# Performance work log

Hardware: AMD Instinct MI355X
Metric: run time of the kernel (lower is better)

The kernel has to match this reference:

```python
import jax, jax.numpy as jnp
import numpy as np

B, T, H = 2, 2048, 1024
NH = 16
HD = H // NH


def setup_inputs() -> dict:
    key = jax.random.key(0)
    ks = jax.random.split(key, 9)
    s = 0.02
    return {
        "x": jax.random.normal(ks[0], (B, T, H), dtype=jnp.float32),
        "attn_mask": jnp.ones((B, T), dtype=jnp.int32),
        "Wq": jax.random.normal(ks[1], (H, H), dtype=jnp.float32) * s,
        "bq": jnp.zeros((H,), dtype=jnp.float32),
        "Wk": jax.random.normal(ks[2], (H, H), dtype=jnp.float32) * s,
        "bk": jnp.zeros((H,), dtype=jnp.float32),
        "Wv": jax.random.normal(ks[3], (H, H), dtype=jnp.float32) * s,
        "bv": jnp.zeros((H,), dtype=jnp.float32),
        "Wo": jax.random.normal(ks[4], (H, H), dtype=jnp.float32) * s,
        "bo": jnp.zeros((H,), dtype=jnp.float32),
    }


def reference(x, attn_mask, Wq, bq, Wk, bk, Wv, bv, Wo, bo):
    Bc, Tc, Hc = x.shape
    scale = HD ** -0.5
    # projections; torch Linear: y = x @ W.T + b (here W stored as [in,out])
    q = (x @ Wq + bq).reshape(Bc, Tc, NH, HD).transpose(0, 2, 1, 3)  # [B,NH,T,HD]
    k = (x @ Wk + bk).reshape(Bc, Tc, NH, HD).transpose(0, 2, 1, 3)
    v = (x @ Wv + bv).reshape(Bc, Tc, NH, HD).transpose(0, 2, 1, 3)
    scores = jnp.einsum('bhqd,bhkd->bhqk', q, k) * scale  # [B,NH,T,T]
    mask = attn_mask.reshape(Bc, 1, 1, Tc)
    scores = jnp.where(mask == 0, jnp.float32(-jnp.inf), scores)
    probs = jax.nn.softmax(scores, axis=-1)
    ctx = jnp.einsum('bhqk,bhkd->bhqd', probs, v)  # [B,NH,T,HD]
    ctx = ctx.transpose(0, 2, 1, 3).reshape(Bc, Tc, Hc)
    out = ctx @ Wo + bo
    return out
```

## Files before the change

### kernel.cpp

```cpp
#include <hip/hip_runtime.h>

typedef _Float16 f16;
typedef _Float16 f16x8 __attribute__((ext_vector_type(8)));
typedef _Float16 f16x4 __attribute__((ext_vector_type(4)));
typedef __fp16 h16x2 __attribute__((ext_vector_type(2)));
typedef float f32x4 __attribute__((ext_vector_type(4)));

#define MFMA32(a, b, c) __builtin_amdgcn_mfma_f32_16x16x32_f16((a), (b), (c), 0, 0, 0)

static constexpr int Bb = 2, T = 2048, H = 1024, NH = 16, HD = 64;
static constexpr int M = Bb * T;
static constexpr int NQKV = 3 * H;
#define QSCALE 0.1803368801111f

__device__ __forceinline__ void gload_lds16(const void* g, void* l) {
  __builtin_amdgcn_global_load_lds(
      (const __attribute__((address_space(1))) void*)g,
      (__attribute__((address_space(3))) void*)l, 16, 0, 0);
}

__global__ __launch_bounds__(256) void pack_all(const float* __restrict__ x,
                                                const float* __restrict__ Wq,
                                                const float* __restrict__ Wk,
                                                const float* __restrict__ Wv,
                                                const float* __restrict__ Wo,
                                                const float* __restrict__ bq,
                                                const float* __restrict__ bk,
                                                const float* __restrict__ bv,
                                                const int* __restrict__ mask,
                                                f16* __restrict__ xh,
                                                f16* __restrict__ WqkvT,
                                                f16* __restrict__ WoT,
                                                float* __restrict__ bqkv,
                                                float* __restrict__ maskf) {
  __shared__ f16 tile[64][65];
  const int bid = blockIdx.x;
  if (bid < 4096) {
    int i = bid * 256 + threadIdx.x;
    float4 v = ((const float4*)x)[i];
    f16x4 o;
    o[0] = (f16)v.x; o[1] = (f16)v.y; o[2] = (f16)v.z; o[3] = (f16)v.w;
    *(f16x4*)(xh + (size_t)i * 4) = o;
  } else if (bid < 5120) {
    int t = bid - 4096;
    int z = t >> 8, rem = t & 255;
    const float* W = (z == 0) ? Wq : (z == 1) ? Wk : (z == 2) ? Wv : Wo;
    f16* Wt = (z < 3) ? (WqkvT + (size_t)z * H * H) : WoT;
    const float scale = (z == 0) ? QSCALE : 1.0f;
    int k0 = (rem >> 4) * 64, n0 = (rem & 15) * 64;
    for (int p = 0; p < 16; ++p) {
      int idx = threadIdx.x + p * 256;
      int r = idx >> 6, c = idx & 63;
      tile[r][c] = (f16)(W[(size_t)(k0 + r) * H + n0 + c] * scale);
    }
    __syncthreads();
    for (int p = 0; p < 16; ++p) {
      int idx = threadIdx.x + p * 256;
      int r = idx >> 6, c = idx & 63;
      Wt[(size_t)(n0 + r) * H + k0 + c] = tile[c][r];
    }
  } else if (bid < 5132) {
    int i = (bid - 5120) * 256 + threadIdx.x;
    if (i < 3072) {
      float v = (i < 1024) ? bq[i] * QSCALE : ((i < 2048) ? bk[i - 1024] : bv[i - 2048]);
      bqkv[i] = v;
    }
  } else {
    int i = (bid - 5132) * 256 + threadIdx.x;
    if (i < Bb * T) maskf[i] = mask[i] ? 1.0f : 0.0f;
  }
}

__global__ __launch_bounds__(256) void vtrans(const f16* __restrict__ QKV,
                                              f16* __restrict__ VT) {
  __shared__ f16 tile[64 * 64];
  const int tid = threadIdx.x;
  const int kv0 = blockIdx.x * 64, h = blockIdx.y, b = blockIdx.z;
  for (int p = 0; p < 2; ++p) {
    int idx = p * 256 + tid;
    int r = idx >> 3, gr = idx & 7;
    f16x8 v = *(const f16x8*)(QKV + (size_t)(b * T + kv0 + r) * NQKV + 2 * H + h * HD + gr * 8);
    *(f16x8*)&tile[r * 64 + (((gr + (r >> 3)) & 7) << 3)] = v;
  }
  __syncthreads();
  const size_t obase = ((size_t)(b * NH + h) * HD) * T;
  for (int p = 0; p < 2; ++p) {
    int idx = p * 256 + tid;
    int d = idx >> 3, kg = idx & 7;
    f16x8 v;
    for (int j = 0; j < 8; ++j) {
      int row = kg * 8 + j;
      v[j] = tile[row * 64 + ((((d >> 3) + kg) & 7) << 3) + (d & 7)];
    }
    int kvr = kv0 + kg * 8;
    int c = (kvr & ~127) | ((kvr + 8 * (d & 15)) & 127);
    *(f16x8*)(VT + obase + (size_t)d * T + c) = v;
  }
}

__device__ __forceinline__ f16x8 lds_frag(const f16* base, int row, int gr) {
  return *(const f16x8*)(base + row * 64 + ((gr ^ (row & 7)) << 3));
}

template <int TM, int TN, bool OUT_F32>
__global__ __launch_bounds__(256, 2) void gemm_f16_bt(const f16* __restrict__ A,
                                                      const f16* __restrict__ Bt,
                                                      const float* __restrict__ bias,
                                                      void* __restrict__ Cout,
                                                      int Nn, int Kk) {
  __shared__ f16 As[2][TM * 64];
  __shared__ f16 Bs[2][TN * 64];
  const int tid = threadIdx.x;
  const int lane = tid & 63, w = tid >> 6;
  const int quad = lane >> 4, l16 = lane & 15;
  const int wm = w >> 1, wn = w & 1;
  const int m0 = blockIdx.y * TM, n0 = blockIdx.x * TN;
  constexpr int AM = TM / 32, AN = TN / 32;

  f32x4 acc[AM][AN];
  for (int a = 0; a < AM; ++a)
    for (int b2 = 0; b2 < AN; ++b2)
      for (int r = 0; r < 4; ++r) acc[a][b2][r] = 0.f;

  auto stage = [&](int k0, int buf) {
    for (int p = 0; p < TM * 8 / 256; ++p) {
      int slot = p * 256 + w * 64 + lane;
      int r = slot >> 3, g = (slot & 7) ^ (r & 7);
      gload_lds16(A + (size_t)(m0 + r) * Kk + k0 + g * 8,
                  (char*)&As[buf][0] + (p * 256 + w * 64) * 16);
    }
    for (int p = 0; p < TN * 8 / 256; ++p) {
      int slot = p * 256 + w * 64 + lane;
      int r = slot >> 3, g = (slot & 7) ^ (r & 7);
      gload_lds16(Bt + (size_t)(n0 + r) * Kk + k0 + g * 8,
                  (char*)&Bs[buf][0] + (p * 256 + w * 64) * 16);
    }
  };

  stage(0, 0);
  __syncthreads();
  const int NIT = Kk / 64;
  for (int it = 0; it < NIT; ++it) {
    const int cur = it & 1;
    if (it + 1 < NIT) stage((it + 1) * 64, cur ^ 1);
    for (int ks = 0; ks < 2; ++ks) {
      f16x8 af[AM], bf[AN];
      for (int t = 0; t < AM; ++t)
        af[t] = lds_frag(&As[cur][0], wm * (TM / 2) + t * 16 + l16, ks * 4 + quad);
      for (int t = 0; t < AN; ++t)
        bf[t] = lds_frag(&Bs[cur][0], wn * (TN / 2) + t * 16 + l16, ks * 4 + quad);
      for (int tm = 0; tm < AM; ++tm)
        for (int tn = 0; tn < AN; ++tn)
          acc[tm][tn] = MFMA32(af[tm], bf[tn], acc[tm][tn]);
    }
    __syncthreads();
  }

  for (int tm = 0; tm < AM; ++tm)
    for (int tn = 0; tn < AN; ++tn)
      for (int r = 0; r < 4; ++r) {
        int m = m0 + wm * (TM / 2) + tm * 16 + quad * 4 + r;
        int n = n0 + wn * (TN / 2) + tn * 16 + l16;
        float v = acc[tm][tn][r] + bias[n];
        if (OUT_F32)
          ((float*)Cout)[(size_t)m * Nn + n] = v;
        else
          ((f16*)Cout)[(size_t)m * Nn + n] = (f16)v;
      }
}


static constexpr int KT_ELE = 128 * 64;
static constexpr int VT_ELE = 64 * 128;

__global__ __launch_bounds__(512, 2) void attn_fused(const f16* __restrict__ QKV,
                                                     const f16* __restrict__ VT,
                                                     const float* __restrict__ maskf,
                                                     f16* __restrict__ ctx) {
  __shared__ __align__(16) char smem[70656];
  f16* KtB = (f16*)smem;
  f16* VtB = (f16*)(smem + 2 * KT_ELE * 2);

  const int tid = threadIdx.x;
  const int w = tid >> 6, lane = tid & 63;
  const int quad = lane >> 4, l16 = lane & 15;
  const int qw = w & 3, g = w >> 2;
  const int q0 = blockIdx.x * 256, h = blockIdx.y, b = blockIdx.z;

  const size_t kbase = (size_t)(b * T) * NQKV + H + h * HD;
  const size_t vtbase = ((size_t)(b * NH + h) * HD) * T;
  const float* maskp = maskf + b * T;

  f16x8 qf[4][2];
  for (int tq = 0; tq < 4; ++tq) {
    const f16* qrow = QKV + (size_t)(b * T + q0 + qw * 64 + tq * 16 + l16) * NQKV + h * HD;
    qf[tq][0] = *(const f16x8*)(qrow + quad * 8);
    qf[tq][1] = *(const f16x8*)(qrow + 32 + quad * 8);
  }

  f32x4 oacc[4][4];
  float lsum[4] = {0.f, 0.f, 0.f, 0.f};
  for (int tq = 0; tq < 4; ++tq)
    for (int t = 0; t < 4; ++t)
      for (int r = 0; r < 4; ++r) oacc[tq][t][r] = 0.f;

  auto stage = [&](int kv0, int buf) {
    f16* Kd = KtB + buf * KT_ELE;
    f16* Vd = VtB + buf * VT_ELE;
    for (int p = 0; p < 2; ++p) {
      int s = p * 512 + tid;
      int R = s >> 3, sg = (s & 7) ^ (R & 7);
      int kv = (R & ~31) | ((R & 12) << 1) | ((R & 16) >> 2) | (R & 3);
      gload_lds16(QKV + kbase + (size_t)(kv0 + kv) * NQKV + sg * 8,
                  (char*)Kd + (p * 512 + w * 64) * 16);
    }
    for (int p = 0; p < 2; ++p) {
      int s = p * 512 + tid;
      int d = s >> 4, cg = s & 15;
      gload_lds16(VT + vtbase + (size_t)d * T + kv0 + cg * 8,
                  (char*)Vd + (p * 512 + w * 64) * 16);
    }
  };

  stage(0, 0);
  __syncthreads();

  for (int it = 0; it < T / 128; ++it) {
    const int cur = it & 1;
    if (it + 1 < T / 128) stage((it + 1) * 128, cur ^ 1);

    const f16* Kc = KtB + cur * KT_ELE;
    const f16* Vc = VtB + cur * VT_ELE;

    for (int s = 0; s < 2; ++s) {
      const int bi = g * 2 + s;
      const int kvabs = it * 128 + bi * 32;
      float4 m0 = *(const float4*)(maskp + kvabs + quad * 8);
      float4 m1 = *(const float4*)(maskp + kvabs + quad * 8 + 4);
      f16x8 kfA0 = lds_frag(Kc, bi * 32 + l16, quad);
      f16x8 kfA1 = lds_frag(Kc, bi * 32 + l16, 4 + quad);
      f16x8 kfB0 = lds_frag(Kc, bi * 32 + 16 + l16, quad);
      f16x8 kfB1 = lds_frag(Kc, bi * 32 + 16 + l16, 4 + quad);
      f16x8 vf[4];
      for (int td = 0; td < 4; ++td)
        vf[td] = *(const f16x8*)&Vc[(td * 16 + l16) * 128 +
                                    ((bi * 32 + quad * 8 + 8 * l16) & 127)];
      for (int tq = 0; tq < 4; ++tq) {
        f32x4 sA = {0.f, 0.f, 0.f, 0.f}, sB = {0.f, 0.f, 0.f, 0.f};
        sA = MFMA32(kfA0, qf[tq][0], sA);
        sA = MFMA32(kfA1, qf[tq][1], sA);
        sB = MFMA32(kfB0, qf[tq][0], sB);
        sB = MFMA32(kfB1, qf[tq][1], sB);
        float pA0 = __builtin_amdgcn_exp2f(sA[0]) * m0.x;
        float pA1 = __builtin_amdgcn_exp2f(sA[1]) * m0.y;
        float pA2 = __builtin_amdgcn_exp2f(sA[2]) * m0.z;
        float pA3 = __builtin_amdgcn_exp2f(sA[3]) * m0.w;
        float pB0 = __builtin_amdgcn_exp2f(sB[0]) * m1.x;
        float pB1 = __builtin_amdgcn_exp2f(sB[1]) * m1.y;
        float pB2 = __builtin_amdgcn_exp2f(sB[2]) * m1.z;
        float pB3 = __builtin_amdgcn_exp2f(sB[3]) * m1.w;
        lsum[tq] += ((pA0 + pA1) + (pA2 + pA3)) + ((pB0 + pB1) + (pB2 + pB3));
        union PF { f16x8 v; h16x2 h[4]; } pf;
        pf.h[0] = __builtin_amdgcn_cvt_pkrtz(pA0, pA1);
        pf.h[1] = __builtin_amdgcn_cvt_pkrtz(pA2, pA3);
        pf.h[2] = __builtin_amdgcn_cvt_pkrtz(pB0, pB1);
        pf.h[3] = __builtin_amdgcn_cvt_pkrtz(pB2, pB3);
        for (int td = 0; td < 4; ++td)
          oacc[tq][td] = MFMA32(vf[td], pf.v, oacc[tq][td]);
      }
    }
    __syncthreads();
  }

  float* cmb = (float*)smem;
  const int slot = qw * 64 + lane;
  if (g == 1) {
    float* dst = cmb + slot * 69;
    int i = 0;
    for (int tq = 0; tq < 4; ++tq)
      for (int td = 0; td < 4; ++td)
        for (int r = 0; r < 4; ++r) dst[i++] = oacc[tq][td][r];
    for (int tq = 0; tq < 4; ++tq) dst[64 + tq] = lsum[tq];
  }
  __syncthreads();
  if (g == 0) {
    const float* src = cmb + slot * 69;
    int i = 0;
    for (int tq = 0; tq < 4; ++tq)
      for (int td = 0; td < 4; ++td)
        for (int r = 0; r < 4; ++r) oacc[tq][td][r] += src[i++];
    for (int tq = 0; tq < 4; ++tq) lsum[tq] += src[64 + tq];

    for (int tq = 0; tq < 4; ++tq) {
      float l = lsum[tq];
      l += __shfl_xor(l, 16, 64);
      l += __shfl_xor(l, 32, 64);
      float inv = 1.f / l;
      int row = b * T + q0 + qw * 64 + tq * 16 + l16;
      for (int td = 0; td < 4; ++td) {
        f16x4 o;
        for (int r = 0; r < 4; ++r) o[r] = (f16)(oacc[tq][td][r] * inv);
        *(f16x4*)(ctx + (size_t)row * H + h * HD + td * 16 + quad * 4) = o;
      }
    }
  }
}


extern "C" void kernel_launch(void* const* d_in, const int* in_sizes, int n_in,
                              void* d_out, int out_size, void* d_ws, size_t ws_size,
                              hipStream_t stream) {
  const float* x  = (const float*)d_in[0];
  const int* mask = (const int*)d_in[1];
  const float* Wq = (const float*)d_in[2];
  const float* bq = (const float*)d_in[3];
  const float* Wk = (const float*)d_in[4];
  const float* bk = (const float*)d_in[5];
  const float* Wv = (const float*)d_in[6];
  const float* bv = (const float*)d_in[7];
  const float* Wo = (const float*)d_in[8];
  const float* bo = (const float*)d_in[9];
  float* out = (float*)d_out;

  char* ws = (char*)d_ws;
  f16* xh      = (f16*)(ws);
  f16* Wqkv_t  = (f16*)(ws + (8u  << 20));
  f16* Wot     = (f16*)(ws + (14u << 20));
  float* bqkv  = (float*)(ws + (16u << 20));
  float* maskf = (float*)(ws + (16u << 20) + 65536);
  f16* QKV     = (f16*)(ws + (17u << 20));
  f16* ctx     = (f16*)(ws + (42u << 20));
  f16* VTr     = (f16*)(ws + (50u << 20));

  pack_all<<<dim3(5164), 256, 0, stream>>>(x, Wq, Wk, Wv, Wo, bq, bk, bv, mask,
                                           xh, Wqkv_t, Wot, bqkv, maskf);

  gemm_f16_bt<128, 128, false><<<dim3(NQKV / 128, M / 128), 256, 0, stream>>>(
      xh, Wqkv_t, bqkv, QKV, NQKV, H);

  vtrans<<<dim3(T / 64, NH, Bb), 256, 0, stream>>>(QKV, VTr);

  attn_fused<<<dim3(T / 256, NH, Bb), 512, 0, stream>>>(QKV, VTr, maskf, ctx);

  gemm_f16_bt<128, 64, true><<<dim3(H / 64, M / 128), 256, 0, stream>>>(
      ctx, Wot, bo, out, H, H);
}
```

Baseline: 195.9 us.

## Fuse V transpose into QKV GEMM epilogue and batch attention MFMAs

The QKV projection GEMM now writes Q/K into a narrower buffer and writes V directly in the transposed, swizzled layout the attention kernel expects, removing the separate vtrans kernel and its extra pass over V. The GEMM tile changes from 128x128 to 128x64 with occupancy hint 3. In the attention inner loop, the score MFMAs for all four query tiles are issued before the exp and PV MFMAs to expose more independent MFMA work. This costs more live registers in attention and produces strided 8-byte stores in the V epilogue.

```diff
diff --git a/kernel.cpp b/kernel.cpp
--- a/kernel.cpp
+++ b/kernel.cpp
@@ -10,7 +10,7 @@
 
 static constexpr int Bb = 2, T = 2048, H = 1024, NH = 16, HD = 64;
 static constexpr int M = Bb * T;
-static constexpr int NQKV = 3 * H;
+static constexpr int NQK = 2 * H;
 #define QSCALE 0.1803368801111f
 
 __device__ __forceinline__ void gload_lds16(const void* g, void* l) {
@@ -71,43 +71,16 @@
   }
 }
 
-__global__ __launch_bounds__(256) void vtrans(const f16* __restrict__ QKV,
-                                              f16* __restrict__ VT) {
-  __shared__ f16 tile[64 * 64];
-  const int tid = threadIdx.x;
-  const int kv0 = blockIdx.x * 64, h = blockIdx.y, b = blockIdx.z;
-  for (int p = 0; p < 2; ++p) {
-    int idx = p * 256 + tid;
-    int r = idx >> 3, gr = idx & 7;
-    f16x8 v = *(const f16x8*)(QKV + (size_t)(b * T + kv0 + r) * NQKV + 2 * H + h * HD + gr * 8);
-    *(f16x8*)&tile[r * 64 + (((gr + (r >> 3)) & 7) << 3)] = v;
-  }
-  __syncthreads();
-  const size_t obase = ((size_t)(b * NH + h) * HD) * T;
-  for (int p = 0; p < 2; ++p) {
-    int idx = p * 256 + tid;
-    int d = idx >> 3, kg = idx & 7;
-    f16x8 v;
-    for (int j = 0; j < 8; ++j) {
-      int row = kg * 8 + j;
-      v[j] = tile[row * 64 + ((((d >> 3) + kg) & 7) << 3) + (d & 7)];
-    }
-    int kvr = kv0 + kg * 8;
-    int c = (kvr & ~127) | ((kvr + 8 * (d & 15)) & 127);
-    *(f16x8*)(VT + obase + (size_t)d * T + c) = v;
-  }
-}
-
 __device__ __forceinline__ f16x8 lds_frag(const f16* base, int row, int gr) {
   return *(const f16x8*)(base + row * 64 + ((gr ^ (row & 7)) << 3));
 }
 
-template <int TM, int TN, bool OUT_F32>
-__global__ __launch_bounds__(256, 2) void gemm_f16_bt(const f16* __restrict__ A,
-                                                      const f16* __restrict__ Bt,
-                                                      const float* __restrict__ bias,
-                                                      void* __restrict__ Cout,
-                                                      int Nn, int Kk) {
+__global__ __launch_bounds__(256, 3) void gemm_qkv(const f16* __restrict__ A,
+                                                   const f16* __restrict__ Bt,
+                                                   const float* __restrict__ bias,
+                                                   f16* __restrict__ QK,
+                                                   f16* __restrict__ VT) {
+  constexpr int TM = 128, TN = 64, Kk = 1024;
   __shared__ f16 As[2][TM * 64];
   __shared__ f16 Bs[2][TN * 64];
   const int tid = threadIdx.x;
@@ -115,21 +88,20 @@
   const int quad = lane >> 4, l16 = lane & 15;
   const int wm = w >> 1, wn = w & 1;
   const int m0 = blockIdx.y * TM, n0 = blockIdx.x * TN;
-  constexpr int AM = TM / 32, AN = TN / 32;
-
-  f32x4 acc[AM][AN];
-  for (int a = 0; a < AM; ++a)
-    for (int b2 = 0; b2 < AN; ++b2)
+
+  f32x4 acc[4][2];
+  for (int a = 0; a < 4; ++a)
+    for (int b2 = 0; b2 < 2; ++b2)
       for (int r = 0; r < 4; ++r) acc[a][b2][r] = 0.f;
 
   auto stage = [&](int k0, int buf) {
-    for (int p = 0; p < TM * 8 / 256; ++p) {
+    for (int p = 0; p < 4; ++p) {
       int slot = p * 256 + w * 64 + lane;
       int r = slot >> 3, g = (slot & 7) ^ (r & 7);
       gload_lds16(A + (size_t)(m0 + r) * Kk + k0 + g * 8,
                   (char*)&As[buf][0] + (p * 256 + w * 64) * 16);
     }
-    for (int p = 0; p < TN * 8 / 256; ++p) {
+    for (int p = 0; p < 2; ++p) {
       int slot = p * 256 + w * 64 + lane;
       int r = slot >> 3, g = (slot & 7) ^ (r & 7);
       gload_lds16(Bt + (size_t)(n0 + r) * Kk + k0 + g * 8,
@@ -139,41 +111,116 @@
 
   stage(0, 0);
   __syncthreads();
-  const int NIT = Kk / 64;
-  for (int it = 0; it < NIT; ++it) {
+  for (int it = 0; it < Kk / 64; ++it) {
     const int cur = it & 1;
-    if (it + 1 < NIT) stage((it + 1) * 64, cur ^ 1);
+    if (it + 1 < Kk / 64) stage((it + 1) * 64, cur ^ 1);
     for (int ks = 0; ks < 2; ++ks) {
-      f16x8 af[AM], bf[AN];
-      for (int t = 0; t < AM; ++t)
-        af[t] = lds_frag(&As[cur][0], wm * (TM / 2) + t * 16 + l16, ks * 4 + quad);
-      for (int t = 0; t < AN; ++t)
-        bf[t] = lds_frag(&Bs[cur][0], wn * (TN / 2) + t * 16 + l16, ks * 4 + quad);
-      for (int tm = 0; tm < AM; ++tm)
-        for (int tn = 0; tn < AN; ++tn)
+      f16x8 af[4], bf[2];
+      for (int t = 0; t < 4; ++t)
+        af[t] = lds_frag(&As[cur][0], wm * 64 + t * 16 + l16, ks * 4 + quad);
+      for (int t = 0; t < 2; ++t)
+        bf[t] = lds_frag(&Bs[cur][0], wn * 32 + t * 16 + l16, ks * 4 + quad);
+      for (int tm = 0; tm < 4; ++tm)
+        for (int tn = 0; tn < 2; ++tn)
           acc[tm][tn] = MFMA32(af[tm], bf[tn], acc[tm][tn]);
     }
     __syncthreads();
   }
 
-  for (int tm = 0; tm < AM; ++tm)
-    for (int tn = 0; tn < AN; ++tn)
+  if (n0 < 2048) {
+    for (int tm = 0; tm < 4; ++tm)
+      for (int tn = 0; tn < 2; ++tn) {
+        int n = n0 + wn * 32 + tn * 16 + l16;
+        float bn = bias[n];
+        for (int r = 0; r < 4; ++r) {
+          int m = m0 + wm * 64 + tm * 16 + quad * 4 + r;
+          QK[(size_t)m * NQK + n] = (f16)(acc[tm][tn][r] + bn);
+        }
+      }
+  } else {
+    for (int tm = 0; tm < 4; ++tm)
+      for (int tn = 0; tn < 2; ++tn) {
+        int ng = n0 + wn * 32 + tn * 16 + l16;
+        float bn = bias[ng];
+        int n = ng - 2048;
+        int h = n >> 6, d = n & 63;
+        int mrow = m0 + wm * 64 + tm * 16 + quad * 4;
+        int bb = mrow >> 11, t = mrow & 2047;
+        int c = (t & ~127) | ((t + 8 * (d & 15)) & 127);
+        f16x4 o;
+        for (int r = 0; r < 4; ++r) o[r] = (f16)(acc[tm][tn][r] + bn);
+        *(f16x4*)(VT + ((size_t)(bb * NH + h) * HD + d) * T + c) = o;
+      }
+  }
+}
+
+__global__ __launch_bounds__(256, 3) void gemm_out(const f16* __restrict__ A,
+                                                   const f16* __restrict__ Bt,
+                                                   const float* __restrict__ bias,
+                                                   float* __restrict__ Cout) {
+  constexpr int TM = 128, TN = 64, Kk = 1024, Nn = 1024;
+  __shared__ f16 As[2][TM * 64];
+  __shared__ f16 Bs[2][TN * 64];
+  const int tid = threadIdx.x;
+  const int lane = tid & 63, w = tid >> 6;
+  const int quad = lane >> 4, l16 = lane & 15;
+  const int wm = w >> 1, wn = w & 1;
+  const int m0 = blockIdx.y * TM, n0 = blockIdx.x * TN;
+
+  f32x4 acc[4][2];
+  for (int a = 0; a < 4; ++a)
+    for (int b2 = 0; b2 < 2; ++b2)
+      for (int r = 0; r < 4; ++r) acc[a][b2][r] = 0.f;
+
+  auto stage = [&](int k0, int buf) {
+    for (int p = 0; p < 4; ++p) {
+      int slot = p * 256 + w * 64 + lane;
+      int r = slot >> 3, g = (slot & 7) ^ (r & 7);
+      gload_lds16(A + (size_t)(m0 + r) * Kk + k0 + g * 8,
+                  (char*)&As[buf][0] + (p * 256 + w * 64) * 16);
+    }
+    for (int p = 0; p < 2; ++p) {
+      int slot = p * 256 + w * 64 + lane;
+      int r = slot >> 3, g = (slot & 7) ^ (r & 7);
+      gload_lds16(Bt + (size_t)(n0 + r) * Kk + k0 + g * 8,
+                  (char*)&Bs[buf][0] + (p * 256 + w * 64) * 16);
+    }
+  };
+
+  stage(0, 0);
+  __syncthreads();
+  for (int it = 0; it < Kk / 64; ++it) {
+    const int cur = it & 1;
+    if (it + 1 < Kk / 64) stage((it + 1) * 64, cur ^ 1);
+    for (int ks = 0; ks < 2; ++ks) {
+      f16x8 af[4], bf[2];
+      for (int t = 0; t < 4; ++t)
+        af[t] = lds_frag(&As[cur][0], wm * 64 + t * 16 + l16, ks * 4 + quad);
+      for (int t = 0; t < 2; ++t)
+        bf[t] = lds_frag(&Bs[cur][0], wn * 32 + t * 16 + l16, ks * 4 + quad);
+      for (int tm = 0; tm < 4; ++tm)
+        for (int tn = 0; tn < 2; ++tn)
+          acc[tm][tn] = MFMA32(af[tm], bf[tn], acc[tm][tn]);
+    }
+    __syncthreads();
+  }
+
+  for (int tm = 0; tm < 4; ++tm)
+    for (int tn = 0; tn < 2; ++tn) {
+      int n = n0 + wn * 32 + tn * 16 + l16;
+      float bn = bias[n];
       for (int r = 0; r < 4; ++r) {
-        int m = m0 + wm * (TM / 2) + tm * 16 + quad * 4 + r;
-        int n = n0 + wn * (TN / 2) + tn * 16 + l16;
-        float v = acc[tm][tn][r] + bias[n];
-        if (OUT_F32)
-          ((float*)Cout)[(size_t)m * Nn + n] = v;
-        else
-          ((f16*)Cout)[(size_t)m * Nn + n] = (f16)v;
-      }
+        int m = m0 + wm * 64 + tm * 16 + quad * 4 + r;
+        Cout[(size_t)m * Nn + n] = acc[tm][tn][r] + bn;
+      }
+    }
 }
 
 
 static constexpr int KT_ELE = 128 * 64;
 static constexpr int VT_ELE = 64 * 128;
 
-__global__ __launch_bounds__(512, 2) void attn_fused(const f16* __restrict__ QKV,
+__global__ __launch_bounds__(512, 2) void attn_fused(const f16* __restrict__ QK,
                                                      const f16* __restrict__ VT,
                                                      const float* __restrict__ maskf,
                                                      f16* __restrict__ ctx) {
@@ -187,13 +234,13 @@
   const int qw = w & 3, g = w >> 2;
   const int q0 = blockIdx.x * 256, h = blockIdx.y, b = blockIdx.z;
 
-  const size_t kbase = (size_t)(b * T) * NQKV + H + h * HD;
+  const size_t kbase = (size_t)(b * T) * NQK + H + h * HD;
   const size_t vtbase = ((size_t)(b * NH + h) * HD) * T;
   const float* maskp = maskf + b * T;
 
   f16x8 qf[4][2];
   for (int tq = 0; tq < 4; ++tq) {
-    const f16* qrow = QKV + (size_t)(b * T + q0 + qw * 64 + tq * 16 + l16) * NQKV + h * HD;
+    const f16* qrow = QK + (size_t)(b * T + q0 + qw * 64 + tq * 16 + l16) * NQK + h * HD;
     qf[tq][0] = *(const f16x8*)(qrow + quad * 8);
     qf[tq][1] = *(const f16x8*)(qrow + 32 + quad * 8);
   }
@@ -211,7 +258,7 @@
       int s = p * 512 + tid;
       int R = s >> 3, sg = (s & 7) ^ (R & 7);
       int kv = (R & ~31) | ((R & 12) << 1) | ((R & 16) >> 2) | (R & 3);
-      gload_lds16(QKV + kbase + (size_t)(kv0 + kv) * NQKV + sg * 8,
+      gload_lds16(QK + kbase + (size_t)(kv0 + kv) * NQK + sg * 8,
                   (char*)Kd + (p * 512 + w * 64) * 16);
     }
     for (int p = 0; p < 2; ++p) {
@@ -245,29 +292,40 @@
       for (int td = 0; td < 4; ++td)
         vf[td] = *(const f16x8*)&Vc[(td * 16 + l16) * 128 +
                                     ((bi * 32 + quad * 8 + 8 * l16) & 127)];
+
+      f32x4 sA[4], sB[4];
       for (int tq = 0; tq < 4; ++tq) {
-        f32x4 sA = {0.f, 0.f, 0.f, 0.f}, sB = {0.f, 0.f, 0.f, 0.f};
-        sA = MFMA32(kfA0, qf[tq][0], sA);
-        sA = MFMA32(kfA1, qf[tq][1], sA);
-        sB = MFMA32(kfB0, qf[tq][0], sB);
-        sB = MFMA32(kfB1, qf[tq][1], sB);
-        float pA0 = __builtin_amdgcn_exp2f(sA[0]) * m0.x;
-        float pA1 = __builtin_amdgcn_exp2f(sA[1]) * m0.y;
-        float pA2 = __builtin_amdgcn_exp2f(sA[2]) * m0.z;
-        float pA3 = __builtin_amdgcn_exp2f(sA[3]) * m0.w;
-        float pB0 = __builtin_amdgcn_exp2f(sB[0]) * m1.x;
-        float pB1 = __builtin_amdgcn_exp2f(sB[1]) * m1.y;
-        float pB2 = __builtin_amdgcn_exp2f(sB[2]) * m1.z;
-        float pB3 = __builtin_amdgcn_exp2f(sB[3]) * m1.w;
+        f32x4 z = {0.f, 0.f, 0.f, 0.f};
+        sA[tq] = MFMA32(kfA0, qf[tq][0], z);
+        sB[tq] = MFMA32(kfB0, qf[tq][0], z);
+      }
+      for (int tq = 0; tq < 4; ++tq) {
+        sA[tq] = MFMA32(kfA1, qf[tq][1], sA[tq]);
+        sB[tq] = MFMA32(kfB1, qf[tq][1], sB[tq]);
+      }
+
+      f16x8 pf[4];
+      for (int tq = 0; tq < 4; ++tq) {
+        float pA0 = __builtin_amdgcn_exp2f(sA[tq][0]) * m0.x;
+        float pA1 = __builtin_amdgcn_exp2f(sA[tq][1]) * m0.y;
+        float pA2 = __builtin_amdgcn_exp2f(sA[tq][2]) * m0.z;
+        float pA3 = __builtin_amdgcn_exp2f(sA[tq][3]) * m0.w;
+        float pB0 = __builtin_amdgcn_exp2f(sB[tq][0]) * m1.x;
+        float pB1 = __builtin_amdgcn_exp2f(sB[tq][1]) * m1.y;
+        float pB2 = __builtin_amdgcn_exp2f(sB[tq][2]) * m1.z;
+        float pB3 = __builtin_amdgcn_exp2f(sB[tq][3]) * m1.w;
         lsum[tq] += ((pA0 + pA1) + (pA2 + pA3)) + ((pB0 + pB1) + (pB2 + pB3));
-        union PF { f16x8 v; h16x2 h[4]; } pf;
-        pf.h[0] = __builtin_amdgcn_cvt_pkrtz(pA0, pA1);
-        pf.h[1] = __builtin_amdgcn_cvt_pkrtz(pA2, pA3);
-        pf.h[2] = __builtin_amdgcn_cvt_pkrtz(pB0, pB1);
-        pf.h[3] = __builtin_amdgcn_cvt_pkrtz(pB2, pB3);
+        union PF { f16x8 v; h16x2 h[4]; } u;
+        u.h[0] = __builtin_amdgcn_cvt_pkrtz(pA0, pA1);
+        u.h[1] = __builtin_amdgcn_cvt_pkrtz(pA2, pA3);
+        u.h[2] = __builtin_amdgcn_cvt_pkrtz(pB0, pB1);
+        u.h[3] = __builtin_amdgcn_cvt_pkrtz(pB2, pB3);
+        pf[tq] = u.v;
+      }
+
+      for (int tq = 0; tq < 4; ++tq)
         for (int td = 0; td < 4; ++td)
-          oacc[tq][td] = MFMA32(vf[td], pf.v, oacc[tq][td]);
-      }
+          oacc[tq][td] = MFMA32(vf[td], pf[tq], oacc[tq][td]);
     }
     __syncthreads();
   }
@@ -328,20 +386,17 @@
   f16* Wot     = (f16*)(ws + (14u << 20));
   float* bqkv  = (float*)(ws + (16u << 20));
   float* maskf = (float*)(ws + (16u << 20) + 65536);
-  f16* QKV     = (f16*)(ws + (17u << 20));
-  f16* ctx     = (f16*)(ws + (42u << 20));
-  f16* VTr     = (f16*)(ws + (50u << 20));
+  f16* QK      = (f16*)(ws + (17u << 20));
+  f16* ctx     = (f16*)(ws + (34u << 20));
+  f16* VTr     = (f16*)(ws + (43u << 20));
 
   pack_all<<<dim3(5164), 256, 0, stream>>>(x, Wq, Wk, Wv, Wo, bq, bk, bv, mask,
                                            xh, Wqkv_t, Wot, bqkv, maskf);
 
-  gemm_f16_bt<128, 128, false><<<dim3(NQKV / 128, M / 128), 256, 0, stream>>>(
-      xh, Wqkv_t, bqkv, QKV, NQKV, H);
-
-  vtrans<<<dim3(T / 64, NH, Bb), 256, 0, stream>>>(QKV, VTr);
-
-  attn_fused<<<dim3(T / 256, NH, Bb), 512, 0, stream>>>(QKV, VTr, maskf, ctx);
-
-  gemm_f16_bt<128, 64, true><<<dim3(H / 64, M / 128), 256, 0, stream>>>(
-      ctx, Wot, bo, out, H, H);
-}
+  gemm_qkv<<<dim3(3 * H / 64, M / 128), 256, 0, stream>>>(
+      xh, Wqkv_t, bqkv, QK, VTr);
+
+  attn_fused<<<dim3(T / 256, NH, Bb), 512, 0, stream>>>(QK, VTr, maskf, ctx);
+
+  gemm_out<<<dim3(H / 64, M / 128), 256, 0, stream>>>(ctx, Wot, bo, out);
+}
```

Result: faster. 191.4 us (-2.3%).
